# Kernel tuning notes

Hardware: AMD Instinct MI355X
Metric: run time of the kernel (lower is better)

The kernel has to match this reference:

```python
import jax, jax.numpy as jnp
import numpy as np

MAX_REL = 127  # default max_relative_position of NEZHA-style RelativePositionsEncoding


def rel_pos_encoding(L, d):
    """Clipped relative-distance sinusoidal encoding, shape [L, L, d]."""
    vocab = 2 * MAX_REL + 1
    pos = np.arange(vocab, dtype=np.float32)[:, None]
    i = np.arange(d)
    div = np.power(10000.0, (2 * (i // 2)) / d).astype(np.float32)
    ang = pos / div
    table = np.where(i % 2 == 0, np.sin(ang), np.cos(ang)).astype(np.float32)  # [vocab, d]
    dist = np.clip(np.arange(L)[None, :] - np.arange(L)[:, None], -MAX_REL, MAX_REL) + MAX_REL
    return jnp.asarray(table[dist])  # [L, L, d]


def setup_inputs() -> dict:
    key = jax.random.key(0)
    ks = jax.random.split(key, 5)
    B, L, H, C = 2, 256, 256, 5
    return {
        "hidden_state": jax.random.normal(ks[0], (B, L, H), dtype=jnp.float32),
        "mask": jnp.ones((B, L), dtype=jnp.int32),
        "Wh_w": jax.random.normal(ks[1], (4 * H, H), dtype=jnp.float32) * 0.02,
        "Wh_b": jax.random.normal(ks[2], (H,), dtype=jnp.float32) * 0.02,
        "Wo_w": jax.random.normal(ks[3], (H, C), dtype=jnp.float32) * 0.02,
        "Wo_b": jax.random.normal(ks[4], (C,), dtype=jnp.float32) * 0.02,
    }


def reference(hidden_state, mask, Wh_w, Wh_b, Wo_w, Wo_b):
    B, L, H = hidden_state.shape
    # Decompose Wh over the concat [end, start, end-start, end*start]:
    # Wh(cat) = end@(We+Wd) + start@(Ws-Wd) + (end*start)@Wm + rel@Wh + b  (exact, linearity)
    We, Ws, Wd, Wm = jnp.split(Wh_w, 4, axis=0)  # each [H, H]
    rel = rel_pos_encoding(L, 4 * H)                        # [L, L, 4H]
    rel_term = jnp.einsum('ijk,kh->ijh', rel, Wh_w)         # [L, L, H]
    a = hidden_state @ (We + Wd)                            # end-index contribution  [B, L, H]
    b = hidden_state @ (Ws - Wd)                            # start-index contribution [B, L, H]
    prod = hidden_state[:, :, None, :] * hidden_state[:, None, :, :]  # [B, L, L, H]
    pre = a[:, :, None, :] + b[:, None, :, :] + prod @ Wm + rel_term[None] + Wh_b
    hij = jnp.tanh(pre)                                     # [B, L, L, H]
    logits = hij @ Wo_w + Wo_b                              # [B, L, L, C]
    logits = jnp.transpose(logits, (0, 3, 1, 2))            # [B, C, L, L]
    m = mask.astype(bool)
    bad = (~m[:, None, :, None]) | (~m[:, None, None, :])
    logits = jnp.where(bad, -jnp.inf, logits)
    tri = jnp.tril(jnp.ones((L, L), logits.dtype), -1) * 1e12
    return logits - tri
```

## Files before the change

kernel.cpp:

```cpp
#include <hip/hip_runtime.h>
#include <math.h>

typedef _Float16 half8 __attribute__((ext_vector_type(8)));
typedef _Float16 half4v __attribute__((ext_vector_type(4)));
typedef float floatx4 __attribute__((ext_vector_type(4)));

union U16 { uint4 u; half8 h; };

__global__ __launch_bounds__(256) void k_prep1(
    const float* __restrict__ hs, const float* __restrict__ Wh,
    const float* __restrict__ Wo,
    float* __restrict__ Rp, float* __restrict__ ap, float* __restrict__ bp,
    uint4* __restrict__ WmT2, uint4* __restrict__ WoPk)
{
  __shared__ __align__(16) char pool[32768];
  int bid = blockIdx.x, tid = threadIdx.x;

  if (bid < 512) {
    float (*tbl)[4] = (float(*)[4])pool;
    int dg = bid >> 3, kq = bid & 7, d0 = dg * 4, k0 = kq * 128;
    for (int idx = tid; idx < 512; idx += 256) {
      int t = idx >> 2, dl = idx & 3;
      int k = k0 + t;
      float e = (float)(k & ~1) * (1.0f / 1024.f);
      float div = powf(10000.f, e);
      float ang = (float)(d0 + dl) / div;
      tbl[t][dl] = (k & 1) ? cosf(ang) : sinf(ang);
    }
    __syncthreads();
    int h = tid;
    float acc[4] = {0, 0, 0, 0};
    for (int kk = 0; kk < 128; ++kk) {
      float wv = Wh[(k0 + kk) * 256 + h];
      float4 tr = *(const float4*)&tbl[kk][0];
      acc[0] = fmaf(tr.x, wv, acc[0]);
      acc[1] = fmaf(tr.y, wv, acc[1]);
      acc[2] = fmaf(tr.z, wv, acc[2]);
      acc[3] = fmaf(tr.w, wv, acc[3]);
    }
#pragma unroll
    for (int dl = 0; dl < 4; ++dl)
      Rp[kq * 65536 + (d0 + dl) * 256 + h] = acc[dl];

  } else if (bid < 1024) {
    float (*xs)[4] = (float(*)[4])pool;
    int g = bid - 512, rg = g >> 2, kq = g & 3;
    int r0 = rg * 4, k0 = kq * 64;
    {
      int r = tid >> 6, kk = tid & 63;
      xs[kk][r] = hs[(size_t)(r0 + r) * 256 + k0 + kk];
    }
    __syncthreads();
    int h = tid;
    float aa[4] = {0, 0, 0, 0}, bb[4] = {0, 0, 0, 0};
    for (int kk = 0; kk < 64; ++kk) {
      int k = k0 + kk;
      float we = Wh[k * 256 + h];
      float wsv = Wh[(256 + k) * 256 + h];
      float wd = Wh[(512 + k) * 256 + h];
      float wA = we + wd, wB = wsv - wd;
      float4 xr = *(const float4*)&xs[kk][0];
      aa[0] = fmaf(xr.x, wA, aa[0]);  bb[0] = fmaf(xr.x, wB, bb[0]);
      aa[1] = fmaf(xr.y, wA, aa[1]);  bb[1] = fmaf(xr.y, wB, bb[1]);
      aa[2] = fmaf(xr.z, wA, aa[2]);  bb[2] = fmaf(xr.z, wB, bb[2]);
      aa[3] = fmaf(xr.w, wA, aa[3]);  bb[3] = fmaf(xr.w, wB, bb[3]);
    }
#pragma unroll
    for (int r = 0; r < 4; ++r) {
      ap[kq * 131072 + (r0 + r) * 256 + h] = aa[r];
      bp[kq * 131072 + (r0 + r) * 256 + h] = bb[r];
    }

  } else if (bid < 1028) {
    _Float16 (*T)[256] = (_Float16(*)[256])pool;
    int q = bid - 1024;
    for (int idx = tid; idx < 16384; idx += 256) {
      int k = idx >> 8, h = idx & 255;
      T[k][h] = (_Float16)Wh[(768 + q * 64 + k) * 256 + h];
    }
    __syncthreads();
    for (int gi = tid; gi < 2048; gi += 256) {
      int kbl = gi >> 8, h = gi & 255;
      U16 v;
#pragma unroll
      for (int e = 0; e < 8; ++e) v.h[e] = T[kbl * 8 + e][h];
      WmT2[(q * 8 + kbl) * 256 + h] = v.u;
    }

  } else {
    for (int gi = tid; gi < 512; gi += 256) {
      int kb = gi >> 4, c = gi & 15;
      U16 v;
#pragma unroll
      for (int e = 0; e < 8; ++e)
        v.h[e] = (c < 5) ? (_Float16)Wo[(kb * 8 + e) * 5 + c] : (_Float16)0.f;
      WoPk[gi] = v.u;
    }
  }
}

__global__ __launch_bounds__(256) void k_prep2(
    const float* __restrict__ Rp, const float* __restrict__ ap,
    const float* __restrict__ bp,
    float* __restrict__ R, float* __restrict__ a, float* __restrict__ bv)
{
  int bid = blockIdx.x, h = threadIdx.x;
  if (bid < 255) {
    int d = bid;
    float s = 0.f;
#pragma unroll
    for (int kq = 0; kq < 8; ++kq) s += Rp[kq * 65536 + d * 256 + h];
    R[d * 256 + h] = s;
  } else {
    int r0 = (bid - 255) * 2;
#pragma unroll
    for (int rr = 0; rr < 2; ++rr) {
      int r = r0 + rr;
      float sa = 0.f, sb = 0.f;
#pragma unroll
      for (int kq = 0; kq < 4; ++kq) {
        sa += ap[kq * 131072 + r * 256 + h];
        sb += bp[kq * 131072 + r * 256 + h];
      }
      a[r * 256 + h] = sa;
      bv[r * 256 + h] = sb;
    }
  }
}

__global__ __launch_bounds__(256, 4) void k_main(
    const float* __restrict__ hs, const int* __restrict__ mask,
    const float* __restrict__ R, const float* __restrict__ a,
    const float* __restrict__ bvec, const float* __restrict__ Whb,
    const uint4* __restrict__ WmT2, const uint4* __restrict__ WoPk,
    const float* __restrict__ Wob, float* __restrict__ out)
{
  __shared__ __align__(16) char smem[34304];
  _Float16 (*As)[264] = (_Float16(*)[264])smem;
  float (*stg)[268] = (float(*)[268])smem;

  int bid = blockIdx.x, tid = threadIdx.x;
  int jt = bid & 3, i = (bid >> 2) & 255, b = bid >> 10;
  int j0 = jt * 64;
  int lane = tid & 63, w = tid >> 6;
  int c16 = lane & 15, quad = lane >> 4;
  const float* hsb = hs + (size_t)b * 65536;

  float av[4];
#pragma unroll
  for (int ht2 = 0; ht2 < 4; ++ht2) {
    int hp = 64 * w + 16 * ht2 + c16;
    av[ht2] = a[((size_t)(b * 256 + i)) * 256 + hp] + Whb[hp];
  }

  floatx4 acc[4][4];
#pragma unroll
  for (int hf = 0; hf < 2; ++hf) {
    int jbase = j0 + hf * 32;
#pragma unroll
    for (int it = 0; it < 8; ++it) {
      int idx = it * 256 + tid;
      int row = idx >> 6;
      int c4 = (idx & 63) << 2;
      int jg = jbase + row;
      int dd = jg - i;
      dd = dd < -127 ? -127 : (dd > 127 ? 127 : dd);
      dd += 127;
      float4 bb = *(const float4*)(bvec + ((size_t)(b * 256 + jg)) * 256 + c4);
      float4 rr = *(const float4*)(R + (size_t)dd * 256 + c4);
      float4 s;
      s.x = bb.x + rr.x; s.y = bb.y + rr.y;
      s.z = bb.z + rr.z; s.w = bb.w + rr.w;
      *(float4*)&stg[row][c4] = s;
    }
    __syncthreads();
#pragma unroll
    for (int jj = 0; jj < 2; ++jj) {
      int jt2 = hf * 2 + jj;
#pragma unroll
      for (int r = 0; r < 4; ++r) {
        int jl32 = jj * 16 + quad * 4 + r;
#pragma unroll
        for (int ht2 = 0; ht2 < 4; ++ht2)
          acc[jt2][ht2][r] = av[ht2] + stg[jl32][64 * w + 16 * ht2 + c16];
      }
    }
    __syncthreads();
  }

  {
    int k8 = (tid & 31) * 8;
    float4 xi0 = *(const float4*)(hsb + i * 256 + k8);
    float4 xi1 = *(const float4*)(hsb + i * 256 + k8 + 4);
    int j = tid >> 5;
#pragma unroll
    for (int s = 0; s < 8; ++s, j += 8) {
      float4 xj0 = *(const float4*)(hsb + (j0 + j) * 256 + k8);
      float4 xj1 = *(const float4*)(hsb + (j0 + j) * 256 + k8 + 4);
      half8 p = {(_Float16)(xi0.x * xj0.x), (_Float16)(xi0.y * xj0.y),
                 (_Float16)(xi0.z * xj0.z), (_Float16)(xi0.w * xj0.w),
                 (_Float16)(xi1.x * xj1.x), (_Float16)(xi1.y * xj1.y),
                 (_Float16)(xi1.z * xj1.z), (_Float16)(xi1.w * xj1.w)};
      *(half8*)(&As[j][k8]) = p;
    }
  }
  __syncthreads();

#pragma unroll 1
  for (int kc = 0; kc < 4; ++kc) {
#pragma unroll
    for (int ks = 0; ks < 2; ++ks) {
      int kb = kc * 8 + ks * 4 + quad;
      U16 bg[4];
#pragma unroll
      for (int ht2 = 0; ht2 < 4; ++ht2)
        bg[ht2].u = WmT2[kb * 256 + 64 * w + 16 * ht2 + c16];
      half8 af[4];
#pragma unroll
      for (int jt2 = 0; jt2 < 4; ++jt2)
        af[jt2] = *(const half8*)(&As[jt2 * 16 + c16][kc * 64 + ks * 32 + quad * 8]);
#pragma unroll
      for (int jt2 = 0; jt2 < 4; ++jt2)
#pragma unroll
        for (int ht2 = 0; ht2 < 4; ++ht2)
          acc[jt2][ht2] = __builtin_amdgcn_mfma_f32_16x16x32_f16(
              af[jt2], bg[ht2].h, acc[jt2][ht2], 0, 0, 0);
    }
  }

  __syncthreads();

#pragma unroll
  for (int jt2 = 0; jt2 < 4; ++jt2) {
#pragma unroll
    for (int ht2 = 0; ht2 < 4; ++ht2) {
      int hp = 64 * w + 16 * ht2 + c16;
#pragma unroll
      for (int r = 0; r < 4; ++r) {
        int jl = jt2 * 16 + quad * 4 + r;
        float x = acc[jt2][ht2][r];
        float e = __expf(2.f * x);
        float t = fmaf(-2.f, __builtin_amdgcn_rcpf(e + 1.f), 1.f);
        As[jl][hp] = (_Float16)t;
      }
    }
  }
  __syncthreads();

  {
    U16 wog[8];
#pragma unroll
    for (int s = 0; s < 8; ++s) wog[s].u = WoPk[(s * 4 + quad) * 16 + c16];
    floatx4 accE = {0.f, 0.f, 0.f, 0.f};
#pragma unroll
    for (int s = 0; s < 8; ++s) {
      half8 ae = *(const half8*)(&As[16 * w + c16][s * 32 + quad * 8]);
      accE = __builtin_amdgcn_mfma_f32_16x16x32_f16(ae, wog[s].h, accE, 0, 0, 0);
    }
    const int* mb = mask + b * 256;
    int mi = mb[i];
    int jg0 = j0 + 16 * w + quad * 4;
    int mj[4];
    *(int4*)mj = *(const int4*)(mb + jg0);
    float wob = (c16 < 5) ? Wob[c16] : 0.f;
    float4 v;
#pragma unroll
    for (int r = 0; r < 4; ++r) {
      int jg = jg0 + r;
      float x = accE[r] + wob;
      if (!(mi && mj[r])) x = -INFINITY;
      if (jg < i) x -= 1e12f;
      ((float*)&v)[r] = x;
    }
    if (c16 < 5)
      *(float4*)(&out[(((size_t)b * 5 + c16) * 256 + i) * 256 + jg0]) = v;
  }
}

extern "C" void kernel_launch(void* const* d_in, const int* in_sizes, int n_in,
                              void* d_out, int out_size, void* d_ws, size_t ws_size,
                              hipStream_t stream) {
  const float* hs   = (const float*)d_in[0];
  const int*   mask = (const int*)d_in[1];
  const float* Wh_w = (const float*)d_in[2];
  const float* Wh_b = (const float*)d_in[3];
  const float* Wo_w = (const float*)d_in[4];
  const float* Wo_b = (const float*)d_in[5];

  char* ws = (char*)d_ws;
  float* R    = (float*)(ws + 0);
  float* a    = (float*)(ws + 262144);
  float* bv   = (float*)(ws + 786432);
  uint4* WmT2 = (uint4*)(ws + 1310720);
  uint4* WoPk = (uint4*)(ws + 1441792);
  float* Rp   = (float*)(ws + 1449984);
  float* ap   = (float*)(ws + 3547136);
  float* bp   = (float*)(ws + 5644288);

  k_prep1<<<1029, 256, 0, stream>>>(hs, Wh_w, Wo_w, Rp, ap, bp, WmT2, WoPk);
  k_prep2<<<511, 256, 0, stream>>>(Rp, ap, bp, R, a, bv);
  k_main<<<2048, 256, 0, stream>>>(hs, mask, R, a, bv, Wh_b, WmT2, WoPk, Wo_b,
                                   (float*)d_out);
}
```

Before: 114.7 us.

## Swap MFMA operands to transpose accumulator layout and drop LDS staging

Swaps the A/B operands of the main MFMA so each lane's four accumulator rows run along the hidden dimension rather than along j. The bias init (a + b + R + Whb) can then be loaded directly from global memory as float4 per lane, removing the shared-memory staging pass and its two barriers. The tanh epilogue also writes packed half4 vectors to LDS instead of scalar halves. Shared memory shrinks to the As tile only, which may improve occupancy. The cost is more redundant global/L2 loads of the bvec and R rows across waves.

```diff
diff --git a/kernel.cpp b/kernel.cpp
--- a/kernel.cpp
+++ b/kernel.cpp
@@ -135,9 +135,7 @@
     const uint4* __restrict__ WmT2, const uint4* __restrict__ WoPk,
     const float* __restrict__ Wob, float* __restrict__ out)
 {
-  __shared__ __align__(16) char smem[34304];
-  _Float16 (*As)[264] = (_Float16(*)[264])smem;
-  float (*stg)[268] = (float(*)[268])smem;
+  __shared__ __align__(16) _Float16 As[64][264];
 
   int bid = blockIdx.x, tid = threadIdx.x;
   int jt = bid & 3, i = (bid >> 2) & 255, b = bid >> 10;
@@ -146,46 +144,34 @@
   int c16 = lane & 15, quad = lane >> 4;
   const float* hsb = hs + (size_t)b * 65536;
 
-  float av[4];
+  float4 av4[4];
 #pragma unroll
   for (int ht2 = 0; ht2 < 4; ++ht2) {
-    int hp = 64 * w + 16 * ht2 + c16;
-    av[ht2] = a[((size_t)(b * 256 + i)) * 256 + hp] + Whb[hp];
-  }
-
+    int h0 = 64 * w + 16 * ht2 + quad * 4;
+    float4 aa = *(const float4*)(a + ((size_t)(b * 256 + i)) * 256 + h0);
+    float4 wb = *(const float4*)(Whb + h0);
+    av4[ht2].x = aa.x + wb.x; av4[ht2].y = aa.y + wb.y;
+    av4[ht2].z = aa.z + wb.z; av4[ht2].w = aa.w + wb.w;
+  }
   floatx4 acc[4][4];
 #pragma unroll
-  for (int hf = 0; hf < 2; ++hf) {
-    int jbase = j0 + hf * 32;
-#pragma unroll
-    for (int it = 0; it < 8; ++it) {
-      int idx = it * 256 + tid;
-      int row = idx >> 6;
-      int c4 = (idx & 63) << 2;
-      int jg = jbase + row;
-      int dd = jg - i;
-      dd = dd < -127 ? -127 : (dd > 127 ? 127 : dd);
-      dd += 127;
-      float4 bb = *(const float4*)(bvec + ((size_t)(b * 256 + jg)) * 256 + c4);
-      float4 rr = *(const float4*)(R + (size_t)dd * 256 + c4);
-      float4 s;
-      s.x = bb.x + rr.x; s.y = bb.y + rr.y;
-      s.z = bb.z + rr.z; s.w = bb.w + rr.w;
-      *(float4*)&stg[row][c4] = s;
-    }
-    __syncthreads();
-#pragma unroll
-    for (int jj = 0; jj < 2; ++jj) {
-      int jt2 = hf * 2 + jj;
-#pragma unroll
-      for (int r = 0; r < 4; ++r) {
-        int jl32 = jj * 16 + quad * 4 + r;
-#pragma unroll
-        for (int ht2 = 0; ht2 < 4; ++ht2)
-          acc[jt2][ht2][r] = av[ht2] + stg[jl32][64 * w + 16 * ht2 + c16];
-      }
-    }
-    __syncthreads();
+  for (int jt2 = 0; jt2 < 4; ++jt2) {
+    int jg = j0 + jt2 * 16 + c16;
+    int dd = jg - i;
+    dd = dd < -127 ? -127 : (dd > 127 ? 127 : dd);
+    dd += 127;
+    const float* bpr = bvec + ((size_t)(b * 256 + jg)) * 256;
+    const float* rpr = R + (size_t)dd * 256;
+#pragma unroll
+    for (int ht2 = 0; ht2 < 4; ++ht2) {
+      int h0 = 64 * w + 16 * ht2 + quad * 4;
+      float4 bb = *(const float4*)(bpr + h0);
+      float4 rr = *(const float4*)(rpr + h0);
+      acc[jt2][ht2][0] = av4[ht2].x + (bb.x + rr.x);
+      acc[jt2][ht2][1] = av4[ht2].y + (bb.y + rr.y);
+      acc[jt2][ht2][2] = av4[ht2].z + (bb.z + rr.z);
+      acc[jt2][ht2][3] = av4[ht2].w + (bb.w + rr.w);
+    }
   }
 
   {
@@ -224,7 +210,7 @@
 #pragma unroll
         for (int ht2 = 0; ht2 < 4; ++ht2)
           acc[jt2][ht2] = __builtin_amdgcn_mfma_f32_16x16x32_f16(
-              af[jt2], bg[ht2].h, acc[jt2][ht2], 0, 0, 0);
+              bg[ht2].h, af[jt2], acc[jt2][ht2], 0, 0, 0);
     }
   }
 
@@ -234,15 +220,15 @@
   for (int jt2 = 0; jt2 < 4; ++jt2) {
 #pragma unroll
     for (int ht2 = 0; ht2 < 4; ++ht2) {
-      int hp = 64 * w + 16 * ht2 + c16;
+      int h0 = 64 * w + 16 * ht2 + quad * 4;
+      half4v t4;
 #pragma unroll
       for (int r = 0; r < 4; ++r) {
-        int jl = jt2 * 16 + quad * 4 + r;
         float x = acc[jt2][ht2][r];
         float e = __expf(2.f * x);
-        float t = fmaf(-2.f, __builtin_amdgcn_rcpf(e + 1.f), 1.f);
-        As[jl][hp] = (_Float16)t;
+        t4[r] = (_Float16)fmaf(-2.f, __builtin_amdgcn_rcpf(e + 1.f), 1.f);
       }
+      *(half4v*)(&As[jt2 * 16 + c16][h0]) = t4;
     }
   }
   __syncthreads();
```

Result: slower. 135.4 us (+18.1%).
